# Kernel optimization log

Measured on AMD Instinct MI355X. Metric: run time of the kernel, lower is better.

## Reference

```python
import jax, jax.numpy as jnp
import numpy as np
from jax import lax

ALPHA = 0.2  # LeakyReLU negative slope


def setup_inputs() -> dict:
    key = jax.random.key(0)
    k1, k2, k3, k4, k5 = jax.random.split(key, 5)
    B, Cin, N, L = 16, 64, 1024, 12
    Cout, Kt = 64, 3
    inp = jax.random.normal(k1, (B, Cin, N, L), dtype=jnp.float32)
    adj = jax.random.normal(k2, (B, N, N), dtype=jnp.float32)
    w0 = jax.random.normal(k3, (Cout, Cin, 1, Kt), dtype=jnp.float32) * (1.0 / np.sqrt(Cin * Kt))
    b0 = jax.random.normal(k4, (Cout,), dtype=jnp.float32) * 0.01
    w1 = jax.random.normal(k5, (1, Cout * L, 1), dtype=jnp.float32) * (1.0 / np.sqrt(Cout * L))
    return {"input": inp, "adj": adj, "w0": w0, "b0": b0, "w1": w1}


def reference(input, adj, w0, b0, w1):
    # conv0: Conv2d(in,out,(1,Kt),padding=(0,1)) -> (B, Cout, N, L)
    x = lax.conv_general_dilated(
        input, w0, window_strides=(1, 1), padding=((0, 0), (1, 1)),
        dimension_numbers=("NCHW", "OIHW", "NCHW"))
    x = x + b0[None, :, None, None]
    B, C, N, L = x.shape
    # permute(0,1,3,2).view(B, C*L, N): channel-major over (C, L)
    x1 = jnp.transpose(x, (0, 1, 3, 2)).reshape(B, C * L, N)
    # conv1 (k=1, no bias) applied twice (original uses conv1 for both f_1 and f_2)
    f = jnp.einsum('bkn,k->bn', x1, w1[0, :, 0])  # (B, N)
    # logits[b,i,j] = f_1[b,0,j] + f_2[b,i,0]
    logits = f[:, None, :] + f[:, :, None]  # (B, N, N)
    z = jnp.where(logits >= 0, logits, ALPHA * logits) + adj
    attention = jax.nn.softmax(z, axis=-1)
    attention = jnp.swapaxes(attention, -1, -2)  # (B, N, N)
    h_prime = jnp.einsum('bcnl,bnq->bcql', x, attention)
    return h_prime, attention
```

## Files before the change

### kernel.cpp

```cpp
#include <hip/hip_runtime.h>
#include <stdint.h>

typedef unsigned short ushort_t;
typedef unsigned int uint_t;

#define B_SZ 16
#define CIN 64
#define COUT 64
#define N_SZ 1024
#define L_SZ 12
#define CL 768
#define ALPHA 0.2f

typedef __bf16 bf16x8 __attribute__((ext_vector_type(8)));
typedef float floatx4 __attribute__((ext_vector_type(4)));

__device__ __forceinline__ ushort_t f2bf(float x) {
    uint_t u = __float_as_uint(x);
    u += 0x7fffu + ((u >> 16) & 1u);
    return (ushort_t)(u >> 16);
}
__device__ __forceinline__ float bf2f(ushort_t h) {
    return __uint_as_float(((uint_t)h) << 16);
}

#define ASYNC16(ldsp, gp)                                                \
    __builtin_amdgcn_global_load_lds(                                    \
        (const __attribute__((address_space(1))) void*)(gp),             \
        (__attribute__((address_space(3))) void*)(ldsp), 16, 0, 0)

__global__ __launch_bounds__(256, 4) void conv_f_kernel(
    const float* __restrict__ inp, const float* __restrict__ w0,
    const float* __restrict__ b0, const float* __restrict__ w1,
    ushort_t* __restrict__ Xt, float* __restrict__ fout)
{
    __shared__ float w0L[64 * 16 * 3];
    __shared__ float w1L[16 * 12];
    __shared__ float fred[256];

    const int n0 = blockIdx.x * 64;
    const int cb = blockIdx.y * 16;
    const int b  = blockIdx.z;
    const int t  = threadIdx.x;
    const int n_l = t & 63, ct = t >> 6;

    for (int idx = t; idx < 3072; idx += 256) {
        const int co_l = idx / 192, rem = idx - co_l * 192;
        const int ci = rem / 3, kt = rem - ci * 3;
        w0L[ci * 48 + co_l * 3 + kt] = w0[cb * 192 + idx];
    }
    if (t < 192) w1L[t] = w1[cb * 12 + t];
    __syncthreads();

    float acc[4][12];
#pragma unroll
    for (int c = 0; c < 4; c++)
#pragma unroll
        for (int l = 0; l < 12; l++) acc[c][l] = 0.f;

    const float* ib = inp + (size_t)b * CIN * N_SZ * L_SZ + (size_t)(n0 + n_l) * 12;

    float4 c0 = *(const float4*)(ib);
    float4 c1 = *(const float4*)(ib + 4);
    float4 c2 = *(const float4*)(ib + 8);

#pragma unroll 4
    for (int ci = 0; ci < 63; ci++) {
        const float* nb = ib + (size_t)(ci + 1) * (N_SZ * L_SZ);
        const float4 x0 = *(const float4*)(nb);
        const float4 x1 = *(const float4*)(nb + 4);
        const float4 x2 = *(const float4*)(nb + 8);
        const float p[12] = {c0.x, c0.y, c0.z, c0.w, c1.x, c1.y, c1.z, c1.w,
                             c2.x, c2.y, c2.z, c2.w};
        const float* wr = &w0L[ci * 48 + ct * 12];
#pragma unroll
        for (int c = 0; c < 4; c++) {
            const float wa = wr[c * 3], wb = wr[c * 3 + 1], wc = wr[c * 3 + 2];
            acc[c][0] = fmaf(p[0], wb, fmaf(p[1], wc, acc[c][0]));
#pragma unroll
            for (int l = 1; l < 11; l++)
                acc[c][l] = fmaf(p[l - 1], wa,
                            fmaf(p[l], wb, fmaf(p[l + 1], wc, acc[c][l])));
            acc[c][11] = fmaf(p[10], wa, fmaf(p[11], wb, acc[c][11]));
        }
        c0 = x0; c1 = x1; c2 = x2;
    }
    {
        const float p[12] = {c0.x, c0.y, c0.z, c0.w, c1.x, c1.y, c1.z, c1.w,
                             c2.x, c2.y, c2.z, c2.w};
        const float* wr = &w0L[63 * 48 + ct * 12];
#pragma unroll
        for (int c = 0; c < 4; c++) {
            const float wa = wr[c * 3], wb = wr[c * 3 + 1], wc = wr[c * 3 + 2];
            acc[c][0] = fmaf(p[0], wb, fmaf(p[1], wc, acc[c][0]));
#pragma unroll
            for (int l = 1; l < 11; l++)
                acc[c][l] = fmaf(p[l - 1], wa,
                            fmaf(p[l], wb, fmaf(p[l + 1], wc, acc[c][l])));
            acc[c][11] = fmaf(p[10], wa, fmaf(p[11], wb, acc[c][11]));
        }
    }

    const int n = n0 + n_l;
    ushort_t* XtB = Xt + (size_t)b * CL * N_SZ + n;
    float fp = 0.f;
#pragma unroll
    for (int c = 0; c < 4; c++) {
        const int co_l = ct * 4 + c;
        const float b0v = b0[cb + co_l];
#pragma unroll
        for (int l = 0; l < 12; l++) {
            const float x = acc[c][l] + b0v;
            fp += x * w1L[co_l * 12 + l];
            XtB[(size_t)((cb + co_l) * 12 + l) * N_SZ] = f2bf(x);
        }
    }
    fred[t] = fp;
    __syncthreads();
    if (t < 64) {
        const float s = fred[t] + fred[t + 64] + fred[t + 128] + fred[t + 192];
        atomicAdd(&fout[b * N_SZ + n0 + t], s);
    }
}

__global__ __launch_bounds__(256) void softmax_kernel(
    const float* __restrict__ adj, const float* __restrict__ f,
    ushort_t* __restrict__ Sb)
{
    __shared__ float smx[4], sms[4];
    const int i = blockIdx.x, b = blockIdx.y, t = threadIdx.x;
    const int lane = t & 63, wv = t >> 6;

    const float* frow = f + b * N_SZ;
    const float fi = frow[i];
    const float4 fj = *(const float4*)(frow + 4 * t);
    const float4 av = *(const float4*)(adj + ((size_t)b * N_SZ + i) * N_SZ + 4 * t);

    float z[4];
    z[0] = fi + fj.x; z[1] = fi + fj.y; z[2] = fi + fj.z; z[3] = fi + fj.w;
#pragma unroll
    for (int k = 0; k < 4; k++) z[k] = (z[k] >= 0.f) ? z[k] : ALPHA * z[k];
    z[0] += av.x; z[1] += av.y; z[2] += av.z; z[3] += av.w;

    float mx = fmaxf(fmaxf(z[0], z[1]), fmaxf(z[2], z[3]));
#pragma unroll
    for (int o = 32; o; o >>= 1) mx = fmaxf(mx, __shfl_xor(mx, o, 64));
    if (lane == 0) smx[wv] = mx;
    __syncthreads();
    mx = fmaxf(fmaxf(smx[0], smx[1]), fmaxf(smx[2], smx[3]));

    float e[4], s = 0.f;
#pragma unroll
    for (int k = 0; k < 4; k++) { e[k] = __expf(z[k] - mx); s += e[k]; }
#pragma unroll
    for (int o = 32; o; o >>= 1) s += __shfl_xor(s, o, 64);
    if (lane == 0) sms[wv] = s;
    __syncthreads();
    s = sms[0] + sms[1] + sms[2] + sms[3];
    const float inv = 1.0f / s;

    const uint_t p0 = (uint_t)f2bf(e[0] * inv) | ((uint_t)f2bf(e[1] * inv) << 16);
    const uint_t p1 = (uint_t)f2bf(e[2] * inv) | ((uint_t)f2bf(e[3] * inv) << 16);
    uint2 pk; pk.x = p0; pk.y = p1;
    *(uint2*)&Sb[((size_t)b * N_SZ + i) * N_SZ + 4 * t] = pk;
}

__global__ __launch_bounds__(256) void att_transpose_kernel(
    const ushort_t* __restrict__ Sb, float* __restrict__ att)
{
    __shared__ float T[64][65];
    const int b = blockIdx.z;
    const int i0 = blockIdx.x * 64, j0 = blockIdx.y * 64;
    const int t = threadIdx.x;

#pragma unroll
    for (int ph = 0; ph < 2; ph++) {
        const int idx = ph * 256 + t;
        const int r = idx >> 3, c8 = (idx & 7) * 8;
        const uint4 v = *(const uint4*)(Sb + ((size_t)b * N_SZ + i0 + r) * N_SZ + j0 + c8);
        T[r][c8 + 0] = bf2f((ushort_t)(v.x & 0xffff));
        T[r][c8 + 1] = bf2f((ushort_t)(v.x >> 16));
        T[r][c8 + 2] = bf2f((ushort_t)(v.y & 0xffff));
        T[r][c8 + 3] = bf2f((ushort_t)(v.y >> 16));
        T[r][c8 + 4] = bf2f((ushort_t)(v.z & 0xffff));
        T[r][c8 + 5] = bf2f((ushort_t)(v.z >> 16));
        T[r][c8 + 6] = bf2f((ushort_t)(v.w & 0xffff));
        T[r][c8 + 7] = bf2f((ushort_t)(v.w >> 16));
    }
    __syncthreads();
#pragma unroll
    for (int ph = 0; ph < 4; ph++) {
        const int idx = ph * 256 + t;
        const int jr = idx >> 4, i4 = (idx & 15) * 4;
        float4 o;
        o.x = T[i4 + 0][jr]; o.y = T[i4 + 1][jr];
        o.z = T[i4 + 2][jr]; o.w = T[i4 + 3][jr];
        *(float4*)(att + ((size_t)b * N_SZ + j0 + jr) * N_SZ + i0 + i4) = o;
    }
}

__global__ __launch_bounds__(256) void gemm2_kernel(
    const ushort_t* __restrict__ Sb, const ushort_t* __restrict__ Xt,
    float* __restrict__ out)
{
    __shared__ ushort_t As[512 * 8];
    __shared__ ushort_t Bs[512 * 8];
    const int b = blockIdx.z;
    const int m0 = blockIdx.x * 128, q0 = blockIdx.y * 128;
    const int t = threadIdx.x;
    const int lane = t & 63, wv = t >> 6;
    const int wq = wv >> 1, wm = wv & 1;
    const int kc = lane >> 4, rr = lane & 15;

    const ushort_t* Sbase = Sb + (size_t)b * N_SZ * N_SZ;
    const ushort_t* Xbase = Xt + (size_t)b * CL * N_SZ;

    floatx4 acc[4][4];
#pragma unroll
    for (int i = 0; i < 4; i++)
#pragma unroll
        for (int j = 0; j < 4; j++) acc[i][j] = (floatx4)0.f;

    for (int k0 = 0; k0 < N_SZ; k0 += 32) {
        __syncthreads();
#pragma unroll
        for (int c = 0; c < 2; c++) {
            const int u = c * 256 + t;
            const int r = u & 127, kcs = u >> 7;
            ASYNC16(&As[u * 8], Sbase + (size_t)(q0 + r) * N_SZ + k0 + kcs * 8);
            ASYNC16(&Bs[u * 8], Xbase + (size_t)(m0 + r) * N_SZ + k0 + kcs * 8);
        }
        __syncthreads();

        bf16x8 af[4], bfr[4];
#pragma unroll
        for (int i = 0; i < 4; i++) {
            af[i]  = *(const bf16x8*)&As[(kc * 128 + wq * 64 + i * 16 + rr) * 8];
            bfr[i] = *(const bf16x8*)&Bs[(kc * 128 + wm * 64 + i * 16 + rr) * 8];
        }
#pragma unroll
        for (int i = 0; i < 4; i++)
#pragma unroll
            for (int j = 0; j < 4; j++)
                acc[i][j] = __builtin_amdgcn_mfma_f32_16x16x32_bf16(
                    af[i], bfr[j], acc[i][j], 0, 0, 0);
    }

#pragma unroll
    for (int j = 0; j < 4; j++) {
        const int m = m0 + wm * 64 + j * 16 + rr;
        const int co = m / 12, l = m - co * 12;
        float* ob = out + (size_t)(b * COUT + co) * (N_SZ * L_SZ) + l;
#pragma unroll
        for (int i = 0; i < 4; i++) {
            const int q = q0 + wq * 64 + i * 16 + kc * 4;
#pragma unroll
            for (int r2 = 0; r2 < 4; r2++)
                ob[(size_t)(q + r2) * 12] = acc[i][j][r2];
        }
    }
}

extern "C" void kernel_launch(void* const* d_in, const int* in_sizes, int n_in,
                              void* d_out, int out_size, void* d_ws, size_t ws_size,
                              hipStream_t stream)
{
    const float* inp = (const float*)d_in[0];
    const float* adj = (const float*)d_in[1];
    const float* w0  = (const float*)d_in[2];
    const float* b0  = (const float*)d_in[3];
    const float* w1  = (const float*)d_in[4];

    float* hprime = (float*)d_out;
    float* att    = hprime + (size_t)B_SZ * COUT * N_SZ * L_SZ;

    char* ws = (char*)d_ws;
    ushort_t* Xt = (ushort_t*)ws;
    ushort_t* Sb = (ushort_t*)(ws + (size_t)25165824);
    float*    fw = (float*)(ws + (size_t)25165824 + 33554432);

    hipMemsetAsync(fw, 0, B_SZ * N_SZ * sizeof(float), stream);
    conv_f_kernel<<<dim3(N_SZ / 64, 4, B_SZ), 256, 0, stream>>>(inp, w0, b0, w1, Xt, fw);
    softmax_kernel<<<dim3(N_SZ, B_SZ), 256, 0, stream>>>(adj, fw, Sb);
    att_transpose_kernel<<<dim3(N_SZ / 64, N_SZ / 64, B_SZ), 256, 0, stream>>>(Sb, att);
    gemm2_kernel<<<dim3(CL / 128, N_SZ / 128, B_SZ), 256, 0, stream>>>(Sb, Xt, hprime);
}
```

Measured before the change: 340.6 us.

## Recast conv as fp16 MFMA GEMM and deepen GEMM K-step

The scalar FMA temporal convolution becomes an implicit GEMM on fp16 MFMA. Shifted copies of the input for the three taps are staged in LDS, so each output column is a 192-deep dot product. Each block now reduces f for whole nodes locally and writes it directly, which removes the memset and the global atomics. Separately, the attention GEMM loads 64-wide K chunks per barrier pair instead of 32, halving the number of syncs at the cost of twice the LDS. The conv inputs are rounded to fp16, which adds precision risk.

```diff
diff --git a/kernel.cpp b/kernel.cpp
--- a/kernel.cpp
+++ b/kernel.cpp
@@ -10,10 +10,14 @@
 #define N_SZ 1024
 #define L_SZ 12
 #define CL 768
+#define NL 12288
+#define PT 96
 #define ALPHA 0.2f
 
 typedef __bf16 bf16x8 __attribute__((ext_vector_type(8)));
 typedef float floatx4 __attribute__((ext_vector_type(4)));
+typedef _Float16 half8 __attribute__((ext_vector_type(8)));
+typedef _Float16 half4 __attribute__((ext_vector_type(4)));
 
 __device__ __forceinline__ ushort_t f2bf(float x) {
     uint_t u = __float_as_uint(x);
@@ -29,97 +33,104 @@
         (const __attribute__((address_space(1))) void*)(gp),             \
         (__attribute__((address_space(3))) void*)(ldsp), 16, 0, 0)
 
-__global__ __launch_bounds__(256, 4) void conv_f_kernel(
+__global__ __launch_bounds__(256, 4) void conv_mfma_kernel(
     const float* __restrict__ inp, const float* __restrict__ w0,
     const float* __restrict__ b0, const float* __restrict__ w1,
     ushort_t* __restrict__ Xt, float* __restrict__ fout)
 {
-    __shared__ float w0L[64 * 16 * 3];
-    __shared__ float w1L[16 * 12];
-    __shared__ float fred[256];
-
-    const int n0 = blockIdx.x * 64;
-    const int cb = blockIdx.y * 16;
-    const int b  = blockIdx.z;
+    __shared__ _Float16 Bs[PT * 200];
+    __shared__ float fredcol[PT];
+
+    const int bx = blockIdx.x;
+    const int b  = blockIdx.y;
     const int t  = threadIdx.x;
-    const int n_l = t & 63, ct = t >> 6;
-
-    for (int idx = t; idx < 3072; idx += 256) {
-        const int co_l = idx / 192, rem = idx - co_l * 192;
-        const int ci = rem / 3, kt = rem - ci * 3;
-        w0L[ci * 48 + co_l * 3 + kt] = w0[cb * 192 + idx];
-    }
-    if (t < 192) w1L[t] = w1[cb * 12 + t];
-    __syncthreads();
-
-    float acc[4][12];
-#pragma unroll
-    for (int c = 0; c < 4; c++)
-#pragma unroll
-        for (int l = 0; l < 12; l++) acc[c][l] = 0.f;
-
-    const float* ib = inp + (size_t)b * CIN * N_SZ * L_SZ + (size_t)(n0 + n_l) * 12;
-
-    float4 c0 = *(const float4*)(ib);
-    float4 c1 = *(const float4*)(ib + 4);
-    float4 c2 = *(const float4*)(ib + 8);
-
-#pragma unroll 4
-    for (int ci = 0; ci < 63; ci++) {
-        const float* nb = ib + (size_t)(ci + 1) * (N_SZ * L_SZ);
-        const float4 x0 = *(const float4*)(nb);
-        const float4 x1 = *(const float4*)(nb + 4);
-        const float4 x2 = *(const float4*)(nb + 8);
-        const float p[12] = {c0.x, c0.y, c0.z, c0.w, c1.x, c1.y, c1.z, c1.w,
-                             c2.x, c2.y, c2.z, c2.w};
-        const float* wr = &w0L[ci * 48 + ct * 12];
-#pragma unroll
-        for (int c = 0; c < 4; c++) {
-            const float wa = wr[c * 3], wb = wr[c * 3 + 1], wc = wr[c * 3 + 2];
-            acc[c][0] = fmaf(p[0], wb, fmaf(p[1], wc, acc[c][0]));
-#pragma unroll
-            for (int l = 1; l < 11; l++)
-                acc[c][l] = fmaf(p[l - 1], wa,
-                            fmaf(p[l], wb, fmaf(p[l + 1], wc, acc[c][l])));
-            acc[c][11] = fmaf(p[10], wa, fmaf(p[11], wb, acc[c][11]));
-        }
-        c0 = x0; c1 = x1; c2 = x2;
-    }
-    {
-        const float p[12] = {c0.x, c0.y, c0.z, c0.w, c1.x, c1.y, c1.z, c1.w,
-                             c2.x, c2.y, c2.z, c2.w};
-        const float* wr = &w0L[63 * 48 + ct * 12];
-#pragma unroll
-        for (int c = 0; c < 4; c++) {
-            const float wa = wr[c * 3], wb = wr[c * 3 + 1], wc = wr[c * 3 + 2];
-            acc[c][0] = fmaf(p[0], wb, fmaf(p[1], wc, acc[c][0]));
-#pragma unroll
-            for (int l = 1; l < 11; l++)
-                acc[c][l] = fmaf(p[l - 1], wa,
-                            fmaf(p[l], wb, fmaf(p[l + 1], wc, acc[c][l])));
-            acc[c][11] = fmaf(p[10], wa, fmaf(p[11], wb, acc[c][11]));
-        }
-    }
-
-    const int n = n0 + n_l;
-    ushort_t* XtB = Xt + (size_t)b * CL * N_SZ + n;
-    float fp = 0.f;
-#pragma unroll
-    for (int c = 0; c < 4; c++) {
-        const int co_l = ct * 4 + c;
-        const float b0v = b0[cb + co_l];
-#pragma unroll
-        for (int l = 0; l < 12; l++) {
-            const float x = acc[c][l] + b0v;
-            fp += x * w1L[co_l * 12 + l];
-            XtB[(size_t)((cb + co_l) * 12 + l) * N_SZ] = f2bf(x);
-        }
-    }
-    fred[t] = fp;
-    __syncthreads();
-    if (t < 64) {
-        const float s = fred[t] + fred[t + 64] + fred[t + 128] + fred[t + 192];
-        atomicAdd(&fout[b * N_SZ + n0 + t], s);
+    const int lane = t & 63, w = t >> 6;
+    const int rr = lane & 15, kc = lane >> 4;
+    const int p0 = bx * PT;
+
+    if (t < PT) fredcol[t] = 0.f;
+
+    const float* ibase = inp + (size_t)b * CIN * NL;
+    const half4 hz = (half4)(_Float16)0.f;
+#pragma unroll
+    for (int i = 0; i < 6; i++) {
+        const int idx = i * 256 + t;
+        const int p = idx % PT;
+        const int cig = idx / PT;
+        const int pg = p0 + p;
+        const int l = pg % 12;
+        const float* src = ibase + (size_t)(cig * 4) * NL + pg;
+        half4 hv;
+        hv[0] = (_Float16)src[0];
+        hv[1] = (_Float16)src[NL];
+        hv[2] = (_Float16)src[2 * NL];
+        hv[3] = (_Float16)src[3 * NL];
+        *(half4*)&Bs[p * 200 + 64 + cig * 4] = hv;
+        if (p + 1 < PT) {
+            half4 v0 = hv; if (l == 11) v0 = hz;
+            *(half4*)&Bs[(p + 1) * 200 + cig * 4] = v0;
+        }
+        if (p >= 1) {
+            half4 v2 = hv; if (l == 0) v2 = hz;
+            *(half4*)&Bs[(p - 1) * 200 + 128 + cig * 4] = v2;
+        }
+    }
+    if (t < 16) *(half4*)&Bs[0 * 200 + t * 4] = hz;
+    else if (t < 32) *(half4*)&Bs[95 * 200 + 128 + (t - 16) * 4] = hz;
+
+    const int co_r = w * 16 + rr;
+    half8 af[6];
+#pragma unroll
+    for (int ch = 0; ch < 6; ch++) {
+        const int kt = ch >> 1;
+        const int ci0 = (ch & 1) * 32 + kc * 8;
+        const float* wp = w0 + co_r * 192 + ci0 * 3 + kt;
+#pragma unroll
+        for (int e = 0; e < 8; e++) af[ch][e] = (_Float16)wp[e * 3];
+    }
+
+    __syncthreads();
+
+    floatx4 acc[6];
+#pragma unroll
+    for (int fp = 0; fp < 6; fp++) acc[fp] = (floatx4)0.f;
+#pragma unroll
+    for (int fp = 0; fp < 6; fp++) {
+        const _Float16* brow = &Bs[(fp * 16 + rr) * 200 + kc * 8];
+#pragma unroll
+        for (int ch = 0; ch < 6; ch++) {
+            const half8 bf = *(const half8*)(brow + ch * 32);
+            acc[fp] = __builtin_amdgcn_mfma_f32_16x16x32_f16(af[ch], bf, acc[fp], 0, 0, 0);
+        }
+    }
+
+    float b0v[4];
+#pragma unroll
+    for (int r = 0; r < 4; r++) b0v[r] = b0[w * 16 + kc * 4 + r];
+
+    ushort_t* XtB = Xt + (size_t)b * CL * N_SZ;
+#pragma unroll
+    for (int fp = 0; fp < 6; fp++) {
+        const int pcol = fp * 16 + rr;
+        const int pg = p0 + pcol;
+        const int n = pg / 12;
+        const int l = pg - n * 12;
+        float fc = 0.f;
+#pragma unroll
+        for (int r = 0; r < 4; r++) {
+            const int co = w * 16 + kc * 4 + r;
+            const float x = acc[fp][r] + b0v[r];
+            fc += x * w1[co * 12 + l];
+            XtB[(size_t)(co * 12 + l) * N_SZ + n] = f2bf(x);
+        }
+        atomicAdd(&fredcol[pcol], fc);
+    }
+    __syncthreads();
+    if (t < 8) {
+        float s = 0.f;
+#pragma unroll
+        for (int j = 0; j < 12; j++) s += fredcol[t * 12 + j];
+        fout[b * N_SZ + bx * 8 + t] = s;
     }
 }
 
@@ -203,8 +214,8 @@
     const ushort_t* __restrict__ Sb, const ushort_t* __restrict__ Xt,
     float* __restrict__ out)
 {
-    __shared__ ushort_t As[512 * 8];
-    __shared__ ushort_t Bs[512 * 8];
+    __shared__ ushort_t As[1024 * 8];
+    __shared__ ushort_t Bs[1024 * 8];
     const int b = blockIdx.z;
     const int m0 = blockIdx.x * 128, q0 = blockIdx.y * 128;
     const int t = threadIdx.x;
@@ -221,10 +232,10 @@
 #pragma unroll
         for (int j = 0; j < 4; j++) acc[i][j] = (floatx4)0.f;
 
-    for (int k0 = 0; k0 < N_SZ; k0 += 32) {
+    for (int k0 = 0; k0 < N_SZ; k0 += 64) {
         __syncthreads();
 #pragma unroll
-        for (int c = 0; c < 2; c++) {
+        for (int c = 0; c < 4; c++) {
             const int u = c * 256 + t;
             const int r = u & 127, kcs = u >> 7;
             ASYNC16(&As[u * 8], Sbase + (size_t)(q0 + r) * N_SZ + k0 + kcs * 8);
@@ -232,18 +243,21 @@
         }
         __syncthreads();
 
-        bf16x8 af[4], bfr[4];
-#pragma unroll
-        for (int i = 0; i < 4; i++) {
-            af[i]  = *(const bf16x8*)&As[(kc * 128 + wq * 64 + i * 16 + rr) * 8];
-            bfr[i] = *(const bf16x8*)&Bs[(kc * 128 + wm * 64 + i * 16 + rr) * 8];
-        }
-#pragma unroll
-        for (int i = 0; i < 4; i++)
-#pragma unroll
-            for (int j = 0; j < 4; j++)
-                acc[i][j] = __builtin_amdgcn_mfma_f32_16x16x32_bf16(
-                    af[i], bfr[j], acc[i][j], 0, 0, 0);
+#pragma unroll
+        for (int kk = 0; kk < 2; kk++) {
+            bf16x8 af[4], bfr[4];
+#pragma unroll
+            for (int i = 0; i < 4; i++) {
+                af[i]  = *(const bf16x8*)&As[((kk * 4 + kc) * 128 + wq * 64 + i * 16 + rr) * 8];
+                bfr[i] = *(const bf16x8*)&Bs[((kk * 4 + kc) * 128 + wm * 64 + i * 16 + rr) * 8];
+            }
+#pragma unroll
+            for (int i = 0; i < 4; i++)
+#pragma unroll
+                for (int j = 0; j < 4; j++)
+                    acc[i][j] = __builtin_amdgcn_mfma_f32_16x16x32_bf16(
+                        af[i], bfr[j], acc[i][j], 0, 0, 0);
+        }
     }
 
 #pragma unroll
@@ -279,8 +293,7 @@
     ushort_t* Sb = (ushort_t*)(ws + (size_t)25165824);
     float*    fw = (float*)(ws + (size_t)25165824 + 33554432);
 
-    hipMemsetAsync(fw, 0, B_SZ * N_SZ * sizeof(float), stream);
-    conv_f_kernel<<<dim3(N_SZ / 64, 4, B_SZ), 256, 0, stream>>>(inp, w0, b0, w1, Xt, fw);
+    conv_mfma_kernel<<<dim3(NL / PT, B_SZ), 256, 0, stream>>>(inp, w0, b0, w1, Xt, fw);
     softmax_kernel<<<dim3(N_SZ, B_SZ), 256, 0, stream>>>(adj, fw, Sb);
     att_transpose_kernel<<<dim3(N_SZ / 64, N_SZ / 64, B_SZ), 256, 0, stream>>>(Sb, att);
     gemm2_kernel<<<dim3(CL / 128, N_SZ / 128, B_SZ), 256, 0, stream>>>(Sb, Xt, hprime);
```

After: 394.0 us. +15.7%, slower.
